# Performance work log

Measured on AMD Instinct MI355X. Metric: run time of the kernel, lower is better.

Reference implementation:

```python
import jax, jax.numpy as jnp
import numpy as np

N_EMBD = 1024
N_HEAD = 16
HEAD_DIM = N_EMBD // N_HEAD


def setup_inputs() -> dict:
    key = jax.random.key(0)
    kx, kq, kk, kv, ko = jax.random.split(key, 5)
    B, T, C = 2, 2048, N_EMBD
    s = 1.0 / np.sqrt(C)
    return {
        "x": jax.random.normal(kx, (B, T, C), dtype=jnp.float32),
        "Wq": jax.random.normal(kq, (C, C), dtype=jnp.float32) * s,
        "Wk": jax.random.normal(kk, (C, C), dtype=jnp.float32) * s,
        "Wv": jax.random.normal(kv, (C, C), dtype=jnp.float32) * s,
        "Wo": jax.random.normal(ko, (C, C), dtype=jnp.float32) * s,
    }


def reference(x, Wq, Wk, Wv, Wo):
    B, T, C = x.shape
    H, D = N_HEAD, HEAD_DIM
    # projections (torch Linear: y = x @ W^T)
    q = (x @ Wq.T).reshape(B, T, H, D).transpose(0, 2, 1, 3)  # [B,H,T,D]
    k = (x @ Wk.T).reshape(B, T, H, D).transpose(0, 2, 1, 3)
    v = (x @ Wv.T).reshape(B, T, H, D).transpose(0, 2, 1, 3)
    scale = 1.0 / np.sqrt(D).astype(np.float32)
    scores = jnp.einsum("bhqd,bhkd->bhqk", q, k) * scale  # [B,H,T,T]
    causal = jnp.tril(jnp.ones((T, T), dtype=bool))
    scores = jnp.where(causal, scores, -jnp.inf)
    attn = jax.nn.softmax(scores, axis=-1)
    y = jnp.einsum("bhqk,bhkd->bhqd", attn, v)  # [B,H,T,D]
    y = y.transpose(0, 2, 1, 3).reshape(B, T, C)
    return y @ Wo.T
```

## Files before the change

kernel.cpp:

```cpp
#include <hip/hip_runtime.h>
#include <hip/hip_bf16.h>
#include <math.h>

#define SEQ   2048
#define CDIM  1024
#define NH    16
#define HD    64

typedef __attribute__((ext_vector_type(8))) short bf16x8;
typedef __attribute__((ext_vector_type(4))) float f32x4;
typedef __attribute__((ext_vector_type(4))) short short4v;

__device__ __forceinline__ short f2bf(float f) {
  unsigned int x = __float_as_uint(f);
  x = (x + 0x7fffu + ((x >> 16) & 1u)) >> 16;
  return (short)x;
}

__global__ void cvt_kernel(const float* __restrict__ src, short* __restrict__ dst, int n4) {
  int i = blockIdx.x * blockDim.x + threadIdx.x;
  if (i >= n4) return;
  float4 v = reinterpret_cast<const float4*>(src)[i];
  short4v o;
  o.x = f2bf(v.x); o.y = f2bf(v.y); o.z = f2bf(v.z); o.w = f2bf(v.w);
  reinterpret_cast<short4v*>(dst)[i] = o;
}

template<int MODE>
__global__ __launch_bounds__(256)
void gemm_bt(const short* __restrict__ A,
             const short* __restrict__ W0, const short* __restrict__ W1, const short* __restrict__ W2,
             short* __restrict__ ob0, short* __restrict__ ob1, short* __restrict__ ob2,
             float* __restrict__ of)
{
  constexpr int K = CDIM;
  const int z = (MODE == 0) ? blockIdx.z : 0;
  const short* W;
  short* outb = nullptr;
  if (MODE == 0) {
    W    = (z == 0) ? W0  : (z == 1) ? W1  : W2;
    outb = (z == 0) ? ob0 : (z == 1) ? ob1 : ob2;
  } else {
    W = W0;
  }
  const int m0 = blockIdx.y * 128;
  const int n0 = blockIdx.x * 128;

  __shared__ short As[128 * 40];
  __shared__ short Bs[128 * 40];

  const int tid  = threadIdx.x;
  const int lane = tid & 63;
  const int wid  = tid >> 6;
  const int wr   = wid >> 1;
  const int wc   = wid & 1;
  const int rl   = lane & 15;
  const int g    = lane >> 4;

  f32x4 acc[4][4];
#pragma unroll
  for (int i = 0; i < 4; ++i)
#pragma unroll
    for (int j = 0; j < 4; ++j)
      acc[i][j] = (f32x4){0.f, 0.f, 0.f, 0.f};

  const int srow = tid >> 2;
  const int scol = (tid & 3) * 8;

  for (int kt = 0; kt < K / 32; ++kt) {
    const int k0 = kt * 32;
    *(bf16x8*)&As[srow * 40 + scol]        = *(const bf16x8*)&A[(size_t)(m0 + srow) * K + k0 + scol];
    *(bf16x8*)&As[(srow + 64) * 40 + scol] = *(const bf16x8*)&A[(size_t)(m0 + srow + 64) * K + k0 + scol];
    *(bf16x8*)&Bs[srow * 40 + scol]        = *(const bf16x8*)&W[(size_t)(n0 + srow) * K + k0 + scol];
    *(bf16x8*)&Bs[(srow + 64) * 40 + scol] = *(const bf16x8*)&W[(size_t)(n0 + srow + 64) * K + k0 + scol];
    __syncthreads();

    bf16x8 af[4], bfr[4];
#pragma unroll
    for (int mi = 0; mi < 4; ++mi)
      af[mi] = *(const bf16x8*)&As[(wr * 64 + mi * 16 + rl) * 40 + g * 8];
#pragma unroll
    for (int nj = 0; nj < 4; ++nj)
      bfr[nj] = *(const bf16x8*)&Bs[(wc * 64 + nj * 16 + rl) * 40 + g * 8];
#pragma unroll
    for (int mi = 0; mi < 4; ++mi)
#pragma unroll
      for (int nj = 0; nj < 4; ++nj)
        acc[mi][nj] = __builtin_amdgcn_mfma_f32_16x16x32_bf16(af[mi], bfr[nj], acc[mi][nj], 0, 0, 0);
    __syncthreads();
  }

#pragma unroll
  for (int mi = 0; mi < 4; ++mi) {
#pragma unroll
    for (int nj = 0; nj < 4; ++nj) {
      const int gmb = m0 + wr * 64 + mi * 16 + g * 4;
      const int gn  = n0 + wc * 64 + nj * 16 + rl;
      if (MODE == 0 && z == 2) {
        short4v pk;
#pragma unroll
        for (int r = 0; r < 4; ++r) pk[r] = f2bf(acc[mi][nj][r]);
        const int b = gmb >> 11, t = gmb & 2047;
        const int h = gn >> 6,  d = gn & 63;
        *(short4v*)&outb[(((size_t)(b * NH + h)) * HD + d) * SEQ + t] = pk;
      } else {
#pragma unroll
        for (int r = 0; r < 4; ++r) {
          const int gm = gmb + r;
          const float val = acc[mi][nj][r];
          if (MODE == 0) {
            const int b = gm >> 11, t = gm & 2047;
            const int h = gn >> 6,  d = gn & 63;
            outb[(((size_t)(b * NH + h)) * SEQ + t) * HD + d] = f2bf(val);
          } else {
            of[(size_t)gm * CDIM + gn] = val;
          }
        }
      }
    }
  }
}

__global__ __launch_bounds__(256)
void attn_kernel(const short* __restrict__ q, const short* __restrict__ k,
                 const short* __restrict__ vt, short* __restrict__ yb)
{
  const int bh  = blockIdx.y;
  const int pp  = blockIdx.x;
  const int jA  = pp;
  const int jB  = 31 - pp;
  const int tid = threadIdx.x;
  const int lane = tid & 63;
  const int wid  = tid >> 6;
  const int rl   = lane & 15;
  const int g    = lane >> 4;

  const short* Qp = q  + (size_t)bh * SEQ * HD;
  const short* Kp = k  + (size_t)bh * SEQ * HD;
  const short* Vp = vt + (size_t)bh * HD * SEQ;

  __shared__ short Ks[64 * 72];
  __shared__ short Vs[64 * 72];
  __shared__ short Ps[4][2][16 * 72];

  const int q0A = jA * 64 + wid * 16;
  const int q0B = jB * 64 + wid * 16;

  bf16x8 qfA[2], qfB[2];
#pragma unroll
  for (int ds = 0; ds < 2; ++ds) {
    qfA[ds] = *(const bf16x8*)&Qp[(size_t)(q0A + rl) * HD + ds * 32 + g * 8];
    qfB[ds] = *(const bf16x8*)&Qp[(size_t)(q0B + rl) * HD + ds * 32 + g * 8];
  }

  f32x4 accA[4], accB[4];
  float mA[4], lA[4], mB[4], lB[4];
#pragma unroll
  for (int r = 0; r < 4; ++r) { mA[r] = -INFINITY; lA[r] = 0.f; mB[r] = -INFINITY; lB[r] = 0.f; }
#pragma unroll
  for (int nt = 0; nt < 4; ++nt) { accA[nt] = (f32x4){0,0,0,0}; accB[nt] = (f32x4){0,0,0,0}; }

  const float scale = 0.125f;
  const int srow = tid >> 3;
  const int scol = (tid & 7) * 8;

  auto process = [&](bf16x8 (&qf)[2], f32x4 (&acc)[4], float (&m_run)[4], float (&l_run)[4],
                     bool diag, short* PsW) {
    f32x4 s_[4];
#pragma unroll
    for (int ct = 0; ct < 4; ++ct) s_[ct] = (f32x4){0, 0, 0, 0};
    __builtin_amdgcn_s_setprio(1);
#pragma unroll
    for (int ct = 0; ct < 4; ++ct)
#pragma unroll
      for (int ds = 0; ds < 2; ++ds) {
        bf16x8 kf = *(const bf16x8*)&Ks[(ct * 16 + rl) * 72 + ds * 32 + g * 8];
        s_[ct] = __builtin_amdgcn_mfma_f32_16x16x32_bf16(qf[ds], kf, s_[ct], 0, 0, 0);
      }
    __builtin_amdgcn_s_setprio(0);

    float pm[4] = {-INFINITY, -INFINITY, -INFINITY, -INFINITY};
#pragma unroll
    for (int ct = 0; ct < 4; ++ct)
#pragma unroll
      for (int r = 0; r < 4; ++r) {
        float sv = s_[ct][r] * scale;
        if (diag) {
          const int lq = wid * 16 + g * 4 + r;
          const int lk = ct * 16 + rl;
          sv = (lk <= lq) ? sv : -INFINITY;
        }
        s_[ct][r] = sv;
        pm[r] = fmaxf(pm[r], sv);
      }
#pragma unroll
    for (int r = 0; r < 4; ++r) {
      pm[r] = fmaxf(pm[r], __shfl_xor(pm[r], 1));
      pm[r] = fmaxf(pm[r], __shfl_xor(pm[r], 2));
      pm[r] = fmaxf(pm[r], __shfl_xor(pm[r], 4));
      pm[r] = fmaxf(pm[r], __shfl_xor(pm[r], 8));
      const float mnew = fmaxf(m_run[r], pm[r]);
      const float f = __expf(m_run[r] - mnew);
      m_run[r] = mnew;
      l_run[r] *= f;
#pragma unroll
      for (int nt = 0; nt < 4; ++nt) acc[nt][r] *= f;
    }

#pragma unroll
    for (int ct = 0; ct < 4; ++ct) {
      const int c = ct * 16 + rl;
#pragma unroll
      for (int r = 0; r < 4; ++r) {
        const float p = __expf(s_[ct][r] - m_run[r]);
        l_run[r] += p;
        PsW[(g * 4 + r) * 72 + c] = f2bf(p);
      }
    }

    __builtin_amdgcn_s_setprio(1);
#pragma unroll
    for (int ks = 0; ks < 2; ++ks) {
      bf16x8 pf = *(const bf16x8*)&PsW[rl * 72 + ks * 32 + g * 8];
#pragma unroll
      for (int nt = 0; nt < 4; ++nt) {
        bf16x8 vf = *(const bf16x8*)&Vs[(nt * 16 + rl) * 72 + ks * 32 + g * 8];
        acc[nt] = __builtin_amdgcn_mfma_f32_16x16x32_bf16(pf, vf, acc[nt], 0, 0, 0);
      }
    }
    __builtin_amdgcn_s_setprio(0);
  };

  auto epilogue = [&](f32x4 (&acc)[4], float (&l_run)[4], int q0w) {
    const int b = bh >> 4, h = bh & 15;
#pragma unroll
    for (int r = 0; r < 4; ++r) {
      float lr = l_run[r];
      lr += __shfl_xor(lr, 1);
      lr += __shfl_xor(lr, 2);
      lr += __shfl_xor(lr, 4);
      lr += __shfl_xor(lr, 8);
      const float inv = 1.0f / lr;
      const int qq = q0w + g * 4 + r;
#pragma unroll
      for (int nt = 0; nt < 4; ++nt)
        yb[((size_t)b * SEQ + qq) * CDIM + h * HD + nt * 16 + rl] = f2bf(acc[nt][r] * inv);
    }
  };

  bf16x8 k0 = *(const bf16x8*)&Kp[(size_t)srow * HD + scol];
  bf16x8 k1 = *(const bf16x8*)&Kp[(size_t)(srow + 32) * HD + scol];
  bf16x8 v0 = *(const bf16x8*)&Vp[(size_t)srow * SEQ + scol];
  bf16x8 v1 = *(const bf16x8*)&Vp[(size_t)(srow + 32) * SEQ + scol];

  for (int t = 0; t <= jB; ++t) {
    __syncthreads();
    *(bf16x8*)&Ks[srow * 72 + scol]        = k0;
    *(bf16x8*)&Ks[(srow + 32) * 72 + scol] = k1;
    *(bf16x8*)&Vs[srow * 72 + scol]        = v0;
    *(bf16x8*)&Vs[(srow + 32) * 72 + scol] = v1;
    __syncthreads();

    if (t < jB) {
      const int kn = (t + 1) * 64;
      k0 = *(const bf16x8*)&Kp[(size_t)(kn + srow) * HD + scol];
      k1 = *(const bf16x8*)&Kp[(size_t)(kn + srow + 32) * HD + scol];
      v0 = *(const bf16x8*)&Vp[(size_t)srow * SEQ + kn + scol];
      v1 = *(const bf16x8*)&Vp[(size_t)(srow + 32) * SEQ + kn + scol];
    }

    process(qfB, accB, mB, lB, t == jB, &Ps[wid][0][0]);
    if (t <= jA)
      process(qfA, accA, mA, lA, t == jA, &Ps[wid][1][0]);
  }

  epilogue(accB, lB, q0B);
  epilogue(accA, lA, q0A);
}

extern "C" void kernel_launch(void* const* d_in, const int* in_sizes, int n_in,
                              void* d_out, int out_size, void* d_ws, size_t ws_size,
                              hipStream_t stream) {
  const float* x  = (const float*)d_in[0];
  const float* Wq = (const float*)d_in[1];
  const float* Wk = (const float*)d_in[2];
  const float* Wv = (const float*)d_in[3];
  const float* Wo = (const float*)d_in[4];
  float* out = (float*)d_out;

  char* ws = (char*)d_ws;
  short* xb  = (short*)(ws);
  short* Wqb = (short*)(ws + ((size_t)8  << 20));
  short* Wkb = (short*)(ws + ((size_t)10 << 20));
  short* Wvb = (short*)(ws + ((size_t)12 << 20));
  short* Wob = (short*)(ws + ((size_t)14 << 20));
  short* qb  = (short*)(ws + ((size_t)16 << 20));
  short* kbp = (short*)(ws + ((size_t)24 << 20));
  short* vtp = (short*)(ws + ((size_t)32 << 20));
  short* yb  = (short*)(ws + ((size_t)40 << 20));

  cvt_kernel<<<4096, 256, 0, stream>>>(x,  xb,  1048576);
  cvt_kernel<<<1024, 256, 0, stream>>>(Wq, Wqb, 262144);
  cvt_kernel<<<1024, 256, 0, stream>>>(Wk, Wkb, 262144);
  cvt_kernel<<<1024, 256, 0, stream>>>(Wv, Wvb, 262144);
  cvt_kernel<<<1024, 256, 0, stream>>>(Wo, Wob, 262144);

  gemm_bt<0><<<dim3(8, 32, 3), 256, 0, stream>>>(xb, Wqb, Wkb, Wvb, qb, kbp, vtp, nullptr);

  attn_kernel<<<dim3(16, 32), 256, 0, stream>>>(qb, kbp, vtp, yb);

  gemm_bt<1><<<dim3(8, 32, 1), 256, 0, stream>>>(yb, Wob, nullptr, nullptr,
                                                 nullptr, nullptr, nullptr, out);
}
```

Baseline: 145.3 us.

## Use direct global-to-LDS loads in GEMM and skip unneeded softmax rescales

The GEMM tile staging now uses global_load_lds to move A and W tiles straight into unpadded LDS, removing the round trip through registers. The online softmax skips the cross-lane max reduction and accumulator rescale when no lane's row max grew. The bf16 conversion is switched to the library intrinsic. Dropping the LDS padding can bring back bank conflicts on fragment reads, and the skip branch adds a wave vote per tile.

```diff
diff --git a/kernel.cpp b/kernel.cpp
--- a/kernel.cpp
+++ b/kernel.cpp
@@ -12,9 +12,13 @@
 typedef __attribute__((ext_vector_type(4))) short short4v;
 
 __device__ __forceinline__ short f2bf(float f) {
-  unsigned int x = __float_as_uint(f);
-  x = (x + 0x7fffu + ((x >> 16) & 1u)) >> 16;
-  return (short)x;
+  return (short)__builtin_bit_cast(unsigned short, __float2bfloat16(f));
+}
+
+__device__ __forceinline__ void glds16(const short* g, short* l) {
+  __builtin_amdgcn_global_load_lds(
+      (const __attribute__((address_space(1))) unsigned int*)g,
+      (__attribute__((address_space(3))) unsigned int*)l, 16, 0, 0);
 }
 
 __global__ void cvt_kernel(const float* __restrict__ src, short* __restrict__ dst, int n4) {
@@ -46,8 +50,8 @@
   const int m0 = blockIdx.y * 128;
   const int n0 = blockIdx.x * 128;
 
-  __shared__ short As[128 * 40];
-  __shared__ short Bs[128 * 40];
+  __shared__ __align__(16) short As[128 * 32];
+  __shared__ __align__(16) short Bs[128 * 32];
 
   const int tid  = threadIdx.x;
   const int lane = tid & 63;
@@ -64,24 +68,25 @@
     for (int j = 0; j < 4; ++j)
       acc[i][j] = (f32x4){0.f, 0.f, 0.f, 0.f};
 
-  const int srow = tid >> 2;
-  const int scol = (tid & 3) * 8;
+  const int lrow = lane >> 2;
+  const int lcol = (lane & 3) * 8;
+  const int arow = wid * 32 + lrow;
 
   for (int kt = 0; kt < K / 32; ++kt) {
     const int k0 = kt * 32;
-    *(bf16x8*)&As[srow * 40 + scol]        = *(const bf16x8*)&A[(size_t)(m0 + srow) * K + k0 + scol];
-    *(bf16x8*)&As[(srow + 64) * 40 + scol] = *(const bf16x8*)&A[(size_t)(m0 + srow + 64) * K + k0 + scol];
-    *(bf16x8*)&Bs[srow * 40 + scol]        = *(const bf16x8*)&W[(size_t)(n0 + srow) * K + k0 + scol];
-    *(bf16x8*)&Bs[(srow + 64) * 40 + scol] = *(const bf16x8*)&W[(size_t)(n0 + srow + 64) * K + k0 + scol];
+    glds16(&A[(size_t)(m0 + arow) * K + k0 + lcol],      &As[(wid * 32) * 32]);
+    glds16(&A[(size_t)(m0 + arow + 16) * K + k0 + lcol], &As[(wid * 32 + 16) * 32]);
+    glds16(&W[(size_t)(n0 + arow) * K + k0 + lcol],      &Bs[(wid * 32) * 32]);
+    glds16(&W[(size_t)(n0 + arow + 16) * K + k0 + lcol], &Bs[(wid * 32 + 16) * 32]);
     __syncthreads();
 
     bf16x8 af[4], bfr[4];
 #pragma unroll
     for (int mi = 0; mi < 4; ++mi)
-      af[mi] = *(const bf16x8*)&As[(wr * 64 + mi * 16 + rl) * 40 + g * 8];
+      af[mi] = *(const bf16x8*)&As[(wr * 64 + mi * 16 + rl) * 32 + g * 8];
 #pragma unroll
     for (int nj = 0; nj < 4; ++nj)
-      bfr[nj] = *(const bf16x8*)&Bs[(wc * 64 + nj * 16 + rl) * 40 + g * 8];
+      bfr[nj] = *(const bf16x8*)&Bs[(wc * 64 + nj * 16 + rl) * 32 + g * 8];
 #pragma unroll
     for (int mi = 0; mi < 4; ++mi)
 #pragma unroll
@@ -193,18 +198,24 @@
         s_[ct][r] = sv;
         pm[r] = fmaxf(pm[r], sv);
       }
-#pragma unroll
-    for (int r = 0; r < 4; ++r) {
-      pm[r] = fmaxf(pm[r], __shfl_xor(pm[r], 1));
-      pm[r] = fmaxf(pm[r], __shfl_xor(pm[r], 2));
-      pm[r] = fmaxf(pm[r], __shfl_xor(pm[r], 4));
-      pm[r] = fmaxf(pm[r], __shfl_xor(pm[r], 8));
-      const float mnew = fmaxf(m_run[r], pm[r]);
-      const float f = __expf(m_run[r] - mnew);
-      m_run[r] = mnew;
-      l_run[r] *= f;
-#pragma unroll
-      for (int nt = 0; nt < 4; ++nt) acc[nt][r] *= f;
+
+    bool need = false;
+#pragma unroll
+    for (int r = 0; r < 4; ++r) need = need || (pm[r] > m_run[r]);
+    if (__any((int)need)) {
+#pragma unroll
+      for (int r = 0; r < 4; ++r) {
+        pm[r] = fmaxf(pm[r], __shfl_xor(pm[r], 1));
+        pm[r] = fmaxf(pm[r], __shfl_xor(pm[r], 2));
+        pm[r] = fmaxf(pm[r], __shfl_xor(pm[r], 4));
+        pm[r] = fmaxf(pm[r], __shfl_xor(pm[r], 8));
+        const float mnew = fmaxf(m_run[r], pm[r]);
+        const float f = __expf(m_run[r] - mnew);
+        m_run[r] = mnew;
+        l_run[r] *= f;
+#pragma unroll
+        for (int nt = 0; nt < 4; ++nt) acc[nt][r] *= f;
+      }
     }
 
 #pragma unroll
```

New measurement: 137.8 us. 5.2% less time.
